# Optimization experiments

Hardware: AMD Instinct MI355X
Metric: run time of the kernel (lower is better)

Reference implementation:

```python
import jax, jax.numpy as jnp
import numpy as np

N = 25000      # nodes
E = 400000     # directed edges (avg degree 16)
FN = 32        # node feature dim
FE = 16        # edge feature dim
H = 16         # hidden_state_size
M = 16         # message_size
ITERS = 3      # mp_iterations


def setup_inputs() -> dict:
    key = jax.random.key(0)
    ks = jax.random.split(key, 16)
    s = 0.1
    return {
        "node_features": jax.random.normal(ks[0], (N, FN), jnp.float32),
        "edge_features": jax.random.normal(ks[1], (E, FE), jnp.float32),
        # Initial dense
        "W_init": jax.random.normal(ks[2], (FN, H), jnp.float32) * s,
        "b_init": jnp.zeros((H,), jnp.float32),
        # edge_net dense: FE -> M*H
        "W_edge": jax.random.normal(ks[3], (FE, M * H), jnp.float32) * s,
        "b_edge": jnp.zeros((M * H,), jnp.float32),
        # GRU (keras default, reset_after=True), input dim 1, units H, gate order z|r|h
        "Wi_gru": jax.random.normal(ks[4], (1, 3 * H), jnp.float32) * s,
        "Wh_gru": jax.random.normal(ks[5], (H, 3 * H), jnp.float32) * s,
        "bi_gru": jnp.zeros((3 * H,), jnp.float32),
        "bh_gru": jnp.zeros((3 * H,), jnp.float32),
        # Readout denses -> 1 output
        "W_ri": jax.random.normal(ks[6], (2 * H, 1), jnp.float32) * s,
        "b_ri": jnp.zeros((1,), jnp.float32),
        "W_rj": jax.random.normal(ks[7], (H, 1), jnp.float32) * s,
        "b_rj": jnp.zeros((1,), jnp.float32),
        # graph structure (directed edges): message to `receivers[e]` from `senders[e]`
        "receivers": jax.random.randint(ks[8], (E,), 0, N, jnp.int32),
        "senders": jax.random.randint(ks[9], (E,), 0, N, jnp.int32),
    }


def _gru_seq(seq, Wi, Wh, bi, bh):
    # seq: [N, T] sequence of scalars per node; keras GRU, reset_after=True, units=H
    n = seq.shape[0]
    xs = seq.T[:, :, None]  # [T, N, 1]
    h0 = jnp.zeros((n, H), seq.dtype)

    def step(h, x_t):
        gx = x_t @ Wi + bi            # [N, 3H]
        gh = h @ Wh + bh              # [N, 3H]
        xz, xr, xh = jnp.split(gx, 3, axis=1)
        hz, hr, hh = jnp.split(gh, 3, axis=1)
        z = jax.nn.sigmoid(xz + hz)
        r = jax.nn.sigmoid(xr + hr)
        hcand = jnp.tanh(xh + r * hh)
        h_new = z * h + (1.0 - z) * hcand
        return h_new, None

    h_final, _ = jax.lax.scan(step, h0, xs)
    return h_final


def reference(node_features, edge_features, W_init, b_init, W_edge, b_edge,
              Wi_gru, Wh_gru, bi_gru, bh_gru, W_ri, b_ri, W_rj, b_rj,
              receivers, senders):
    # Initial hidden state
    hidden0 = node_features @ W_init + b_init   # [N, H]
    hidden = hidden0

    # edge_net(edge) reshaped to per-edge matrices [E, M, H] (constant across iterations)
    edge_mats = (edge_features @ W_edge + b_edge).reshape(E, M, H)

    for _ in range(ITERS):
        h_nb = hidden[senders]                                  # [E, H]
        msg = jnp.einsum("emh,eh->em", edge_mats, h_nb)        # [E, M] matvec per edge
        messages = jax.ops.segment_sum(msg, receivers, num_segments=N)  # sum aggregation
        seq = jnp.concatenate([hidden, messages], axis=1)       # [N, H+M]
        hidden = _gru_seq(seq, Wi_gru, Wh_gru, bi_gru, bh_gru)  # [N, H]

    # Readout
    i = jnp.concatenate([hidden, hidden0], axis=1) @ W_ri + b_ri  # [N, 1]
    j = hidden @ W_rj + b_rj                                      # [N, 1]
    return jnp.sum(i * j, axis=0)                                 # [1]
```

## Files before the change

### kernel.cpp

```cpp
#include <hip/hip_runtime.h>

#define N_NODES 25000
#define N_EDGES 400000

__device__ __forceinline__ float fast_sigmoid(float x) {
    return __builtin_amdgcn_rcpf(1.0f + __expf(-x));
}
__device__ __forceinline__ float fast_tanh(float x) {
    return 1.0f - 2.0f * __builtin_amdgcn_rcpf(__expf(2.0f * x) + 1.0f);
}

#define SWZF(x, k) __int_as_float(__builtin_amdgcn_ds_swizzle(__float_as_int(x), ((k) << 10) | 0x1F))
#define BCAST16(x, t) __int_as_float(__builtin_amdgcn_ds_swizzle(__float_as_int(x), ((t) << 5) | 0x10))

__global__ void __launch_bounds__(256) k_init(
        const float* __restrict__ nf, const float* __restrict__ Wini,
        const float* __restrict__ bini,
        float* __restrict__ hidden0, float* __restrict__ hid,
        int* __restrict__ cnt, int* __restrict__ rcnt)
{
    int gtid = blockIdx.x * 256 + threadIdx.x;
    if (gtid <= N_NODES) { cnt[gtid] = 0; rcnt[gtid] = 0; }
    int node = gtid >> 4;
    int j = gtid & 15;
    if (node >= N_NODES) return;

    const float4* nf4 = (const float4*)(nf + node * 32);
    float acc = bini[j];
#pragma unroll
    for (int g = 0; g < 8; ++g) {
        float4 v = nf4[g];
        acc = fmaf(v.x, Wini[(g*4+0)*16 + j], acc);
        acc = fmaf(v.y, Wini[(g*4+1)*16 + j], acc);
        acc = fmaf(v.z, Wini[(g*4+2)*16 + j], acc);
        acc = fmaf(v.w, Wini[(g*4+3)*16 + j], acc);
    }
    hidden0[node*16 + j] = acc;
    hid[node*16 + j] = acc;
}

__global__ void __launch_bounds__(256) k_rank(const int* __restrict__ send,
        const int* __restrict__ recv,
        int* __restrict__ cnt, int* __restrict__ rcnt,
        int* __restrict__ rank_s, int* __restrict__ rank_r)
{
    int e = blockIdx.x * 256 + threadIdx.x;
    if (e < N_EDGES) {
        rank_s[e] = atomicAdd(&cnt[send[e]], 1);
        rank_r[e] = atomicAdd(&rcnt[recv[e]], 1);
    }
}

#define SCAN_TOT 25600
__global__ void __launch_bounds__(1024) k_scan2(
        const int* __restrict__ cnt,  int* __restrict__ row_ptr,
        const int* __restrict__ rcnt, int* __restrict__ rrow_ptr,
        float* __restrict__ out)
{
    __shared__ int data[SCAN_TOT];
    __shared__ int sums[1024];
    int t = threadIdx.x;
    const int CH = 25;

    const int* SRC = blockIdx.x ? rcnt : cnt;
    int* DST = blockIdx.x ? rrow_ptr : row_ptr;

    for (int i = t; i < SCAN_TOT; i += 1024)
        data[i] = (i < N_NODES) ? SRC[i] : 0;
    __syncthreads();

    int base = t * CH;
    int s = 0;
#pragma unroll
    for (int i = 0; i < CH; ++i) s += data[base + i];
    sums[t] = s;
    __syncthreads();

    for (int off = 1; off < 1024; off <<= 1) {
        int add = (t >= off) ? sums[t - off] : 0;
        __syncthreads();
        sums[t] += add;
        __syncthreads();
    }
    int run = sums[t] - s;

#pragma unroll
    for (int i = 0; i < CH; ++i) {
        int v = data[base + i];
        data[base + i] = run;
        run += v;
    }
    __syncthreads();

    for (int i = t; i < N_NODES; i += 1024)
        DST[i] = data[i];
    if (t == 0) {
        if (blockIdx.x == 0) { row_ptr[N_NODES] = N_EDGES; out[0] = 0.0f; }
        else                 { rrow_ptr[N_NODES] = N_EDGES; }
    }
}

__global__ void __launch_bounds__(256) k_place(const int* __restrict__ send,
        const int* __restrict__ recv,
        const int* __restrict__ rank_s, const int* __restrict__ rank_r,
        const int* __restrict__ row_ptr, const int* __restrict__ rrow_ptr,
        int* __restrict__ ipos, int* __restrict__ rp)
{
    int e = blockIdx.x * 256 + threadIdx.x;
    if (e < N_EDGES) {
        int pos = row_ptr[send[e]] + rank_s[e];
        ipos[e] = pos;
        rp[pos] = rrow_ptr[recv[e]] + rank_r[e];
    }
}

__global__ void __launch_bounds__(256) k_permute(const float* __restrict__ ef,
        const int* __restrict__ ipos, float* __restrict__ efp)
{
    int gtid = blockIdx.x * 256 + threadIdx.x;
    int e = gtid >> 4;
    int c = gtid & 15;
    if (e < N_EDGES) efp[(size_t)ipos[e]*16 + c] = ef[(size_t)e*16 + c];
}

#define MCHUNK 512
#define MSG16(E0,E1,E2,E3) ( \
    ( fmaf((E0).w,q[3],  fmaf((E0).z,q[2],  fmaf((E0).y,q[1],  fmaf((E0).x,q[0],  qb)))) \
    + fmaf((E1).w,q[7],  fmaf((E1).z,q[6],  fmaf((E1).y,q[5],  fmaf((E1).x,q[4],  0.0f)))) ) \
  + ( fmaf((E2).w,q[11], fmaf((E2).z,q[10], fmaf((E2).y,q[9],  fmaf((E2).x,q[8],  0.0f)))) \
    + fmaf((E3).w,q[15], fmaf((E3).z,q[14], fmaf((E3).y,q[13], fmaf((E3).x,q[12], 0.0f)))) ) )

__global__ void __launch_bounds__(256) k_msg(
        const float* __restrict__ hid, const float* __restrict__ efp,
        const int* __restrict__ rp,
        const float* __restrict__ We, const float* __restrict__ be,
        const int* __restrict__ row_ptr,
        float* __restrict__ tmp)
{
    __shared__ float sef[MCHUNK * 16];
    __shared__ int   srp[MCHUNK];
    int tid = threadIdx.x;
    int grp = tid >> 4;
    int m   = tid & 15;
    int s   = blockIdx.x * 16 + grp;
    bool active = (s < N_NODES);
    int sc = active ? s : 0;

    int s0 = blockIdx.x * 16;
    int blk_beg = row_ptr[s0];
    int s1 = s0 + 16; if (s1 > N_NODES) s1 = N_NODES;
    int blk_end = row_ptr[s1];

    int beg = active ? row_ptr[s]     : 0;
    int end = active ? row_ptr[s + 1] : 0;

    float h[16];
    {
        const float4* h4 = (const float4*)(hid + sc*16);
        float4 a = h4[0], b = h4[1], c = h4[2], d = h4[3];
        h[0]=a.x; h[1]=a.y; h[2]=a.z;  h[3]=a.w;
        h[4]=b.x; h[5]=b.y; h[6]=b.z;  h[7]=b.w;
        h[8]=c.x; h[9]=c.y; h[10]=c.z; h[11]=c.w;
        h[12]=d.x; h[13]=d.y; h[14]=d.z; h[15]=d.w;
    }
    float q[16];
#pragma unroll
    for (int f = 0; f < 16; ++f) {
        const float4* wf = (const float4*)(We + f*256 + m*16);
        float4 a = wf[0], b = wf[1], c = wf[2], d = wf[3];
        float acc;
        acc  = a.x*h[0]  + a.y*h[1]  + a.z*h[2]  + a.w*h[3];
        acc += b.x*h[4]  + b.y*h[5]  + b.z*h[6]  + b.w*h[7];
        acc += c.x*h[8]  + c.y*h[9]  + c.z*h[10] + c.w*h[11];
        acc += d.x*h[12] + d.y*h[13] + d.z*h[14] + d.w*h[15];
        q[f] = acc;
    }
    float qb;
    {
        const float4* bf = (const float4*)(be + m*16);
        float4 a = bf[0], b = bf[1], c = bf[2], d = bf[3];
        qb  = a.x*h[0]  + a.y*h[1]  + a.z*h[2]  + a.w*h[3];
        qb += b.x*h[4]  + b.y*h[5]  + b.z*h[6]  + b.w*h[7];
        qb += c.x*h[8]  + c.y*h[9]  + c.z*h[10] + c.w*h[11];
        qb += d.x*h[12] + d.y*h[13] + d.z*h[14] + d.w*h[15];
    }

    for (int cbeg = blk_beg; cbeg < blk_end; cbeg += MCHUNK) {
        int cend = cbeg + MCHUNK; if (cend > blk_end) cend = blk_end;
        int nedge = cend - cbeg;
        int nfl = nedge * 4;
        __syncthreads();
        {
            const float4* gsrc = (const float4*)(efp + (size_t)cbeg * 16);
            float4* ldst = (float4*)sef;
            for (int i = tid; i < nfl; i += 256) ldst[i] = gsrc[i];
            for (int i = tid; i < nedge; i += 256) srp[i] = rp[cbeg + i];
        }
        __syncthreads();

        int lo = beg > cbeg ? beg : cbeg;
        int hi = end < cend ? end : cend;
        int i = lo;
        for (; i + 2 <= hi; i += 2) {
            const float4* l0 = (const float4*)(sef + (size_t)(i   - cbeg) * 16);
            const float4* l1 = (const float4*)(sef + (size_t)(i+1 - cbeg) * 16);
            float4 A0=l0[0], A1=l0[1], A2=l0[2], A3=l0[3];
            float4 B0=l1[0], B1=l1[1], B2=l1[2], B3=l1[3];
            int r0 = srp[i   - cbeg];
            int r1 = srp[i+1 - cbeg];
            float v0 = MSG16(A0, A1, A2, A3);
            float v1 = MSG16(B0, B1, B2, B3);
            tmp[(size_t)r0*16 + m] = v0;
            tmp[(size_t)r1*16 + m] = v1;
        }
        for (; i < hi; ++i) {
            const float4* l0 = (const float4*)(sef + (size_t)(i - cbeg) * 16);
            float4 A0=l0[0], A1=l0[1], A2=l0[2], A3=l0[3];
            int r0 = srp[i - cbeg];
            tmp[(size_t)r0*16 + m] = MSG16(A0, A1, A2, A3);
        }
    }
}

__global__ void __launch_bounds__(256) k_gru(
        const float* __restrict__ hid_in, const float* __restrict__ tmp,
        const int* __restrict__ rrow_ptr,
        const float* __restrict__ Wi, const float* __restrict__ Wh,
        const float* __restrict__ bi, const float* __restrict__ bh,
        float* __restrict__ hid_out)
{
    int gtid = blockIdx.x * 256 + threadIdx.x;
    int node = gtid >> 4;
    int j = gtid & 15;
    if (node >= N_NODES) return;

    float s0 = 0.0f, s1 = 0.0f, s2 = 0.0f, s3 = 0.0f;
    {
        int beg = rrow_ptr[node];
        int end = rrow_ptr[node + 1];
        const float* p = tmp + (size_t)beg * 16 + j;
        int d = end - beg;
        int i = 0;
        for (; i + 8 <= d; i += 8) {
            float a0 = p[(i+0)*16];
            float a1 = p[(i+1)*16];
            float a2 = p[(i+2)*16];
            float a3 = p[(i+3)*16];
            float a4 = p[(i+4)*16];
            float a5 = p[(i+5)*16];
            float a6 = p[(i+6)*16];
            float a7 = p[(i+7)*16];
            s0 += a0; s1 += a1; s2 += a2; s3 += a3;
            s0 += a4; s1 += a5; s2 += a6; s3 += a7;
        }
        for (; i < d; ++i) s0 += p[i*16];
    }
    float msg_own = (s0 + s1) + (s2 + s3);
    float h_own = hid_in[node*16 + j];

    float Wz[16], Wr[16], Wc[16];
#pragma unroll
    for (int k = 0; k < 16; ++k) {
        int l = j ^ k;
        Wz[k] = Wh[l*48 + j];
        Wr[k] = Wh[l*48 + 16 + j];
        Wc[k] = Wh[l*48 + 32 + j];
    }
    float Wiz = Wi[j], Wir = Wi[16+j], Wih = Wi[32+j];
    float cz   = bi[j] + bh[j];
    float cr   = bi[16+j] + bh[16+j];
    float bih_ = bi[32+j];
    float bhh_ = bh[32+j];

    float hn = 0.0f;

#define STEPK(k) { float v = SWZF(hn, k); \
        az = fmaf(v, Wz[k], az); ar = fmaf(v, Wr[k], ar); ac = fmaf(v, Wc[k], ac); }

#define GRUSTEP(XV) { \
        float xv = (XV); \
        float az = fmaf(xv, Wiz, cz); \
        float ar = fmaf(xv, Wir, cr); \
        float ac = bhh_; \
        az = fmaf(hn, Wz[0], az); \
        ar = fmaf(hn, Wr[0], ar); \
        ac = fmaf(hn, Wc[0], ac); \
        STEPK(1)  STEPK(2)  STEPK(3)  STEPK(4)  STEPK(5) \
        STEPK(6)  STEPK(7)  STEPK(8)  STEPK(9)  STEPK(10) \
        STEPK(11) STEPK(12) STEPK(13) STEPK(14) STEPK(15) \
        float z  = fast_sigmoid(az); \
        float r  = fast_sigmoid(ar); \
        float hc = fast_tanh(fmaf(xv, Wih, bih_) + r * ac); \
        hn = fmaf(z, hn - hc, hc); }

    GRUSTEP(BCAST16(h_own, 0))  GRUSTEP(BCAST16(h_own, 1))
    GRUSTEP(BCAST16(h_own, 2))  GRUSTEP(BCAST16(h_own, 3))
    GRUSTEP(BCAST16(h_own, 4))  GRUSTEP(BCAST16(h_own, 5))
    GRUSTEP(BCAST16(h_own, 6))  GRUSTEP(BCAST16(h_own, 7))
    GRUSTEP(BCAST16(h_own, 8))  GRUSTEP(BCAST16(h_own, 9))
    GRUSTEP(BCAST16(h_own, 10)) GRUSTEP(BCAST16(h_own, 11))
    GRUSTEP(BCAST16(h_own, 12)) GRUSTEP(BCAST16(h_own, 13))
    GRUSTEP(BCAST16(h_own, 14)) GRUSTEP(BCAST16(h_own, 15))
    GRUSTEP(BCAST16(msg_own, 0))  GRUSTEP(BCAST16(msg_own, 1))
    GRUSTEP(BCAST16(msg_own, 2))  GRUSTEP(BCAST16(msg_own, 3))
    GRUSTEP(BCAST16(msg_own, 4))  GRUSTEP(BCAST16(msg_own, 5))
    GRUSTEP(BCAST16(msg_own, 6))  GRUSTEP(BCAST16(msg_own, 7))
    GRUSTEP(BCAST16(msg_own, 8))  GRUSTEP(BCAST16(msg_own, 9))
    GRUSTEP(BCAST16(msg_own, 10)) GRUSTEP(BCAST16(msg_own, 11))
    GRUSTEP(BCAST16(msg_own, 12)) GRUSTEP(BCAST16(msg_own, 13))
    GRUSTEP(BCAST16(msg_own, 14)) GRUSTEP(BCAST16(msg_own, 15))
#undef GRUSTEP
#undef STEPK

    hid_out[node*16 + j] = hn;
}

__global__ void __launch_bounds__(256) k_readout(
        const float* __restrict__ hid, const float* __restrict__ hid0,
        const float* __restrict__ Wri, const float* __restrict__ bri,
        const float* __restrict__ Wrj, const float* __restrict__ brj,
        float* __restrict__ out)
{
    int n = blockIdx.x * 256 + threadIdx.x;
    float val = 0.0f;
    if (n < N_NODES) {
        const float4* h4 = (const float4*)(hid + n * 16);
        const float4* g4 = (const float4*)(hid0 + n * 16);
        float iv = bri[0];
        float jv = brj[0];
#pragma unroll
        for (int g = 0; g < 4; ++g) {
            float4 h  = h4[g];
            float4 h0 = g4[g];
            iv = fmaf(h.x,  Wri[g*4+0], iv);  iv = fmaf(h.y,  Wri[g*4+1], iv);
            iv = fmaf(h.z,  Wri[g*4+2], iv);  iv = fmaf(h.w,  Wri[g*4+3], iv);
            iv = fmaf(h0.x, Wri[16+g*4+0], iv); iv = fmaf(h0.y, Wri[16+g*4+1], iv);
            iv = fmaf(h0.z, Wri[16+g*4+2], iv); iv = fmaf(h0.w, Wri[16+g*4+3], iv);
            jv = fmaf(h.x,  Wrj[g*4+0], jv);  jv = fmaf(h.y,  Wrj[g*4+1], jv);
            jv = fmaf(h.z,  Wrj[g*4+2], jv);  jv = fmaf(h.w,  Wrj[g*4+3], jv);
        }
        val = iv * jv;
    }
#pragma unroll
    for (int off = 32; off > 0; off >>= 1)
        val += __shfl_xor(val, off, 64);
    __shared__ float wsum[4];
    int w = threadIdx.x >> 6;
    if ((threadIdx.x & 63) == 0) wsum[w] = val;
    __syncthreads();
    if (threadIdx.x == 0)
        atomicAdd(out, wsum[0] + wsum[1] + wsum[2] + wsum[3]);
}

extern "C" void kernel_launch(void* const* d_in, const int* in_sizes, int n_in,
                              void* d_out, int out_size, void* d_ws, size_t ws_size,
                              hipStream_t stream)
{
    const float* node_features = (const float*)d_in[0];
    const float* edge_features = (const float*)d_in[1];
    const float* W_init = (const float*)d_in[2];
    const float* b_init = (const float*)d_in[3];
    const float* W_edge = (const float*)d_in[4];
    const float* b_edge = (const float*)d_in[5];
    const float* Wi_gru = (const float*)d_in[6];
    const float* Wh_gru = (const float*)d_in[7];
    const float* bi_gru = (const float*)d_in[8];
    const float* bh_gru = (const float*)d_in[9];
    const float* W_ri = (const float*)d_in[10];
    const float* b_ri = (const float*)d_in[11];
    const float* W_rj = (const float*)d_in[12];
    const float* b_rj = (const float*)d_in[13];
    const int* receivers = (const int*)d_in[14];
    const int* senders   = (const int*)d_in[15];
    float* out = (float*)d_out;

    float* fb      = (float*)d_ws;
    float* hidden0 = fb;
    float* hidA    = fb + 400000;
    float* hidB    = fb + 800000;
    float* tmp     = fb + 1200000;
    float* efp     = fb + 7600000;
    int* ib       = (int*)(fb + 14000000);
    int* cnt      = ib;
    int* row_ptr  = ib + 25024;
    int* rcnt     = ib + 50048;
    int* rrow_ptr = ib + 75072;
    int* ipos     = ib + 100096;
    int* rp       = ib + 500096;
    int* rank_s   = ib + 900096;
    int* rank_r   = ib + 1300096;

    dim3 b256(256);
    int grid_n16 = (N_NODES * 16 + 255) / 256;
    int grid_e   = (N_EDGES + 255) / 256;
    int grid_e16 = (N_EDGES * 16 + 255) / 256;
    int grid_n   = (N_NODES + 255) / 256;
    int grid_blk = (N_NODES + 15) / 16;

    k_init<<<grid_n16, b256, 0, stream>>>(node_features, W_init, b_init,
                                          hidden0, hidA, cnt, rcnt);
    k_rank<<<grid_e, b256, 0, stream>>>(senders, receivers, cnt, rcnt,
                                        rank_s, rank_r);
    k_scan2<<<2, 1024, 0, stream>>>(cnt, row_ptr, rcnt, rrow_ptr, out);
    k_place<<<grid_e, b256, 0, stream>>>(senders, receivers, rank_s, rank_r,
                                         row_ptr, rrow_ptr, ipos, rp);
    k_permute<<<grid_e16, b256, 0, stream>>>(edge_features, ipos, efp);

    float* hin = hidA;
    float* hout = hidB;
    for (int it = 0; it < 3; ++it) {
        k_msg<<<grid_blk, b256, 0, stream>>>(hin, efp, rp,
                                             W_edge, b_edge, row_ptr, tmp);
        k_gru<<<grid_n16, b256, 0, stream>>>(hin, tmp, rrow_ptr,
                                             Wi_gru, Wh_gru, bi_gru, bh_gru, hout);
        float* t = hin; hin = hout; hout = t;
    }

    k_readout<<<grid_n, b256, 0, stream>>>(hin, hidden0, W_ri, b_ri, W_rj, b_rj, out);
}
```

Baseline: 405.3 us.

## Fuse edge-feature permutation into placement kernel and split GRU accumulator chains

The separate permute kernel is folded into k_place, so each edge thread copies its 16 features with float4 loads and stores straight to the sorted position. This drops the ipos array, one kernel launch and an extra round trip through memory. Separately, the GRU recurrence now keeps two independent accumulator chains per gate, which halves the serial FMA dependency depth in each of the 32 steps. The cost is a few extra registers and adds, and the float summation order changes slightly.

```diff
diff --git a/kernel.cpp b/kernel.cpp
--- a/kernel.cpp
+++ b/kernel.cpp
@@ -104,23 +104,18 @@
         const int* __restrict__ recv,
         const int* __restrict__ rank_s, const int* __restrict__ rank_r,
         const int* __restrict__ row_ptr, const int* __restrict__ rrow_ptr,
-        int* __restrict__ ipos, int* __restrict__ rp)
+        const float* __restrict__ ef, float* __restrict__ efp,
+        int* __restrict__ rp)
 {
     int e = blockIdx.x * 256 + threadIdx.x;
     if (e < N_EDGES) {
         int pos = row_ptr[send[e]] + rank_s[e];
-        ipos[e] = pos;
         rp[pos] = rrow_ptr[recv[e]] + rank_r[e];
-    }
-}
-
-__global__ void __launch_bounds__(256) k_permute(const float* __restrict__ ef,
-        const int* __restrict__ ipos, float* __restrict__ efp)
-{
-    int gtid = blockIdx.x * 256 + threadIdx.x;
-    int e = gtid >> 4;
-    int c = gtid & 15;
-    if (e < N_EDGES) efp[(size_t)ipos[e]*16 + c] = ef[(size_t)e*16 + c];
+        const float4* src = (const float4*)(ef + (size_t)e * 16);
+        float4* dst = (float4*)(efp + (size_t)pos * 16);
+        float4 a = src[0], b = src[1], c = src[2], d = src[3];
+        dst[0] = a; dst[1] = b; dst[2] = c; dst[3] = d;
+    }
 }
 
 #define MCHUNK 512
@@ -274,23 +269,30 @@
 
     float hn = 0.0f;
 
-#define STEPK(k) { float v = SWZF(hn, k); \
-        az = fmaf(v, Wz[k], az); ar = fmaf(v, Wr[k], ar); ac = fmaf(v, Wc[k], ac); }
+#define STEPK2(k0, k1) { \
+        float va = SWZF(hn, k0); float vb = SWZF(hn, k1); \
+        az0 = fmaf(va, Wz[k0], az0); az1 = fmaf(vb, Wz[k1], az1); \
+        ar0 = fmaf(va, Wr[k0], ar0); ar1 = fmaf(vb, Wr[k1], ar1); \
+        ac0 = fmaf(va, Wc[k0], ac0); ac1 = fmaf(vb, Wc[k1], ac1); }
 
 #define GRUSTEP(XV) { \
         float xv = (XV); \
-        float az = fmaf(xv, Wiz, cz); \
-        float ar = fmaf(xv, Wir, cr); \
-        float ac = bhh_; \
-        az = fmaf(hn, Wz[0], az); \
-        ar = fmaf(hn, Wr[0], ar); \
-        ac = fmaf(hn, Wc[0], ac); \
-        STEPK(1)  STEPK(2)  STEPK(3)  STEPK(4)  STEPK(5) \
-        STEPK(6)  STEPK(7)  STEPK(8)  STEPK(9)  STEPK(10) \
-        STEPK(11) STEPK(12) STEPK(13) STEPK(14) STEPK(15) \
-        float z  = fast_sigmoid(az); \
-        float r  = fast_sigmoid(ar); \
-        float hc = fast_tanh(fmaf(xv, Wih, bih_) + r * ac); \
+        float v1 = SWZF(hn, 1); \
+        float az0 = fmaf(xv, Wiz, cz); \
+        float ar0 = fmaf(xv, Wir, cr); \
+        float ac0 = bhh_; \
+        az0 = fmaf(hn, Wz[0], az0); \
+        ar0 = fmaf(hn, Wr[0], ar0); \
+        ac0 = fmaf(hn, Wc[0], ac0); \
+        float az1 = v1 * Wz[1]; \
+        float ar1 = v1 * Wr[1]; \
+        float ac1 = v1 * Wc[1]; \
+        STEPK2(2,3)   STEPK2(4,5)   STEPK2(6,7) \
+        STEPK2(8,9)   STEPK2(10,11) STEPK2(12,13) \
+        STEPK2(14,15) \
+        float z  = fast_sigmoid(az0 + az1); \
+        float r  = fast_sigmoid(ar0 + ar1); \
+        float hc = fast_tanh(fmaf(xv, Wih, bih_) + r * (ac0 + ac1)); \
         hn = fmaf(z, hn - hc, hc); }
 
     GRUSTEP(BCAST16(h_own, 0))  GRUSTEP(BCAST16(h_own, 1))
@@ -310,7 +312,7 @@
     GRUSTEP(BCAST16(msg_own, 12)) GRUSTEP(BCAST16(msg_own, 13))
     GRUSTEP(BCAST16(msg_own, 14)) GRUSTEP(BCAST16(msg_own, 15))
 #undef GRUSTEP
-#undef STEPK
+#undef STEPK2
 
     hid_out[node*16 + j] = hn;
 }
@@ -385,15 +387,13 @@
     int* row_ptr  = ib + 25024;
     int* rcnt     = ib + 50048;
     int* rrow_ptr = ib + 75072;
-    int* ipos     = ib + 100096;
-    int* rp       = ib + 500096;
-    int* rank_s   = ib + 900096;
-    int* rank_r   = ib + 1300096;
+    int* rp       = ib + 100096;
+    int* rank_s   = ib + 500096;
+    int* rank_r   = ib + 900096;
 
     dim3 b256(256);
     int grid_n16 = (N_NODES * 16 + 255) / 256;
     int grid_e   = (N_EDGES + 255) / 256;
-    int grid_e16 = (N_EDGES * 16 + 255) / 256;
     int grid_n   = (N_NODES + 255) / 256;
     int grid_blk = (N_NODES + 15) / 16;
 
@@ -403,8 +403,8 @@
                                         rank_s, rank_r);
     k_scan2<<<2, 1024, 0, stream>>>(cnt, row_ptr, rcnt, rrow_ptr, out);
     k_place<<<grid_e, b256, 0, stream>>>(senders, receivers, rank_s, rank_r,
-                                         row_ptr, rrow_ptr, ipos, rp);
-    k_permute<<<grid_e16, b256, 0, stream>>>(edge_features, ipos, efp);
+                                         row_ptr, rrow_ptr,
+                                         edge_features, efp, rp);
 
     float* hin = hidA;
     float* hout = hidB;
```

Measured after the change: 402.5 us. Within noise of the previous version (-0.7%).
